# Kernel tuning notes

Measured on AMD Instinct MI355X. Metric: run time of the kernel, lower is better.

Reference implementation:

```python
import jax, jax.numpy as jnp
import numpy as np

VAL_CONF = 0.1
NUM_CLASSES = 80
IMG_SIZE = 608.0


def setup_inputs() -> dict:
    key = jax.random.key(0)
    bs, H, W = 16, 76, 76
    num_mask, attrs = 3, 5 + NUM_CLASSES
    x = jax.random.normal(key, (bs, num_mask * attrs, H, W), dtype=jnp.float32)
    # scaled anchors (anchor_px / img_size) for mask [0,1,2] of YOLOv3 @ 608
    anchors = jnp.array([[10.0, 13.0], [16.0, 30.0], [33.0, 23.0]], dtype=jnp.float32) / IMG_SIZE
    return {"x": x, "anchors": anchors}


def reference(x, anchors):
    # x: [bs, num_mask*(5+nc), H, W]; anchors: [num_mask, 2] (scaled)
    bs, C, H, W = x.shape
    nm = anchors.shape[0]
    attrs = C // nm
    a = x.reshape(bs, nm, attrs, H, W)

    xy = jax.nn.sigmoid(a[:, :, 0:2])          # tx, ty  [bs,nm,2,H,W]
    wh = jnp.exp(a[:, :, 2:4])                 # tw, th
    conf = jax.nn.sigmoid(a[:, :, 4])          # objectness [bs,nm,H,W]
    cls = jax.nn.sigmoid(a[:, :, 5:])          # class probs [bs,nm,nc,H,W]

    gx = jnp.arange(W, dtype=x.dtype)[None, None, None, :]
    gy = jnp.arange(H, dtype=x.dtype)[None, None, :, None]

    cx = (xy[:, :, 0] + gx) / W                # normalized center x
    cy = (xy[:, :, 1] + gy) / H
    bw = wh[:, :, 0] * anchors[None, :, 0, None, None]
    bh = wh[:, :, 1] * anchors[None, :, 1, None, None]

    cls_score = jnp.max(cls, axis=2)           # [bs,nm,H,W]
    cls_idx = jnp.argmax(cls, axis=2).astype(x.dtype)

    # [bs, nm, H, W, 7]: x1,y1,x2,y2,conf,cls_score,cls_idx
    pred = jnp.stack(
        [cx - bw * 0.5, cy - bh * 0.5, cx + bw * 0.5, cy + bh * 0.5,
         conf, cls_score, cls_idx], axis=-1)

    # fixed-shape replacement for the conf>val_conf boolean filter + cat
    valid = conf > VAL_CONF                    # [bs,nm,H,W] bool
    pred = pred * valid[..., None].astype(x.dtype)
    return pred, valid
```

## Files before the change

kernel.cpp:

```cpp
#include <hip/hip_runtime.h>


#define BS    16
#define NM    3
#define NC    80
#define ATTRS (5 + NC)
#define HH    76
#define WW    76
#define HWSZ  (HH * WW)
#define VAL_CONF 0.1f

__device__ __forceinline__ float sigmoidf(float v) {
    return 1.0f / (1.0f + __expf(-v));
}

__global__ __launch_bounds__(256) void yolo_head_kernel(
    const float* __restrict__ x,
    const float* __restrict__ anchors,
    float* __restrict__ out) {

    const int tid = blockIdx.x * blockDim.x + threadIdx.x;

    const int bm = tid / HWSZ;
    const int hw = tid - bm * HWSZ;
    const int m  = bm % NM;

    const float aw = anchors[2 * m + 0];
    const float ah = anchors[2 * m + 1];

    const float* base = x + (size_t)bm * ATTRS * HWSZ + hw;

    const float tx = base[0 * HWSZ];
    const float ty = base[1 * HWSZ];
    const float tw = base[2 * HWSZ];
    const float th = base[3 * HWSZ];
    const float tc = base[4 * HWSZ];

    float mx = base[5 * HWSZ];
    int   mi = 0;
    #pragma unroll
    for (int k = 1; k < NC; ++k) {
        const float c = base[(size_t)(5 + k) * HWSZ];
        if (c > mx) { mx = c; mi = k; }
    }

    const int h = hw / WW;
    const int w = hw - h * WW;

    const float sx = sigmoidf(tx);
    const float sy = sigmoidf(ty);
    const float cx = (sx + (float)w) * (1.0f / (float)WW);
    const float cy = (sy + (float)h) * (1.0f / (float)HH);
    const float bw = __expf(tw) * aw;
    const float bh = __expf(th) * ah;
    const float conf      = sigmoidf(tc);
    const float cls_score = sigmoidf(mx);
    const float cls_idx   = (float)mi;

    const float fm = (conf > VAL_CONF) ? 1.0f : 0.0f;

    float* pred = out + (size_t)tid * 7;
    pred[0] = (cx - bw * 0.5f) * fm;
    pred[1] = (cy - bh * 0.5f) * fm;
    pred[2] = (cx + bw * 0.5f) * fm;
    pred[3] = (cy + bh * 0.5f) * fm;
    pred[4] = conf * fm;
    pred[5] = cls_score * fm;
    pred[6] = cls_idx * fm;

    out[(size_t)BS * NM * HWSZ * 7 + tid] = fm;
}

extern "C" void kernel_launch(void* const* d_in, const int* in_sizes, int n_in,
                              void* d_out, int out_size, void* d_ws, size_t ws_size,
                              hipStream_t stream) {
    const float* x       = (const float*)d_in[0];
    const float* anchors = (const float*)d_in[1];
    float* out           = (float*)d_out;

    const int total = BS * NM * HWSZ;
    const int block = 256;
    const int grid  = total / block;

    yolo_head_kernel<<<grid, block, 0, stream>>>(x, anchors, out);
}
```

Before: 21.95 us.

## Split class argmax across 4-lane groups with float4 loads and shuffle reduce

Each group of four threads now covers four adjacent spatial positions. Each thread loads float4 vectors from a strided subset of the 80 class planes, so it handles 20 classes for all four positions. Partial max/argmax values are then combined with xor shuffles, ties going to the lower index. The aim is fewer, wider load instructions per thread and fewer dependent compares, at the cost of shuffle overhead and extra registers.

```diff
diff --git a/kernel.cpp b/kernel.cpp
--- a/kernel.cpp
+++ b/kernel.cpp
@@ -10,6 +10,8 @@
 #define HWSZ  (HH * WW)
 #define VAL_CONF 0.1f
 
+typedef float f4 __attribute__((ext_vector_type(4)));
+
 __device__ __forceinline__ float sigmoidf(float v) {
     return 1.0f / (1.0f + __expf(-v));
 }
@@ -19,33 +21,56 @@
     const float* __restrict__ anchors,
     float* __restrict__ out) {
 
-    const int tid = blockIdx.x * blockDim.x + threadIdx.x;
+    const int gtid = blockIdx.x * blockDim.x + threadIdx.x;
+    const int t    = gtid & 3;
+    const int e0   = gtid & ~3;
 
-    const int bm = tid / HWSZ;
-    const int hw = tid - bm * HWSZ;
-    const int m  = bm % NM;
+    const int bm  = e0 / HWSZ;
+    const int hw0 = e0 - bm * HWSZ;
+    const int m   = bm % NM;
 
     const float aw = anchors[2 * m + 0];
     const float ah = anchors[2 * m + 1];
 
-    const float* base = x + (size_t)bm * ATTRS * HWSZ + hw;
+    const float* base = x + (size_t)bm * (ATTRS * HWSZ) + hw0;
 
-    const float tx = base[0 * HWSZ];
-    const float ty = base[1 * HWSZ];
-    const float tw = base[2 * HWSZ];
-    const float th = base[3 * HWSZ];
-    const float tc = base[4 * HWSZ];
+    const float tx = base[0 * HWSZ + t];
+    const float ty = base[1 * HWSZ + t];
+    const float tw = base[2 * HWSZ + t];
+    const float th = base[3 * HWSZ + t];
+    const float tc = base[4 * HWSZ + t];
 
-    float mx = base[5 * HWSZ];
-    int   mi = 0;
+    f4  mx = *(const f4*)(base + (size_t)(5 + t) * HWSZ);
+    int mi[4] = {t, t, t, t};
+
     #pragma unroll
-    for (int k = 1; k < NC; ++k) {
-        const float c = base[(size_t)(5 + k) * HWSZ];
-        if (c > mx) { mx = c; mi = k; }
+    for (int i = 1; i < NC / 4; ++i) {
+        const int k = t + 4 * i;
+        const f4 c = *(const f4*)(base + (size_t)(5 + k) * HWSZ);
+        #pragma unroll
+        for (int j = 0; j < 4; ++j) {
+            if (c[j] > mx[j]) { mx[j] = c[j]; mi[j] = k; }
+        }
     }
 
-    const int h = hw / WW;
-    const int w = hw - h * WW;
+    #pragma unroll
+    for (int d = 1; d <= 2; d <<= 1) {
+        #pragma unroll
+        for (int j = 0; j < 4; ++j) {
+            const float omx = __shfl_xor(mx[j], d);
+            const int   omi = __shfl_xor(mi[j], d);
+            if (omx > mx[j] || (omx == mx[j] && omi < mi[j])) {
+                mx[j] = omx; mi[j] = omi;
+            }
+        }
+    }
+
+    const float mxv = (t == 0) ? mx[0] : (t == 1) ? mx[1] : (t == 2) ? mx[2] : mx[3];
+    const int   miv = (t == 0) ? mi[0] : (t == 1) ? mi[1] : (t == 2) ? mi[2] : mi[3];
+
+    const int hw = hw0 + t;
+    const int h  = hw / WW;
+    const int w  = hw - h * WW;
 
     const float sx = sigmoidf(tx);
     const float sy = sigmoidf(ty);
@@ -54,12 +79,12 @@
     const float bw = __expf(tw) * aw;
     const float bh = __expf(th) * ah;
     const float conf      = sigmoidf(tc);
-    const float cls_score = sigmoidf(mx);
-    const float cls_idx   = (float)mi;
+    const float cls_score = sigmoidf(mxv);
+    const float cls_idx   = (float)miv;
 
     const float fm = (conf > VAL_CONF) ? 1.0f : 0.0f;
 
-    float* pred = out + (size_t)tid * 7;
+    float* pred = out + (size_t)gtid * 7;
     pred[0] = (cx - bw * 0.5f) * fm;
     pred[1] = (cy - bh * 0.5f) * fm;
     pred[2] = (cx + bw * 0.5f) * fm;
@@ -68,7 +93,7 @@
     pred[5] = cls_score * fm;
     pred[6] = cls_idx * fm;
 
-    out[(size_t)BS * NM * HWSZ * 7 + tid] = fm;
+    out[(size_t)BS * NM * HWSZ * 7 + gtid] = fm;
 }
 
 extern "C" void kernel_launch(void* const* d_in, const int* in_sizes, int n_in,
```

Result: slower. 22.63 us (+3.1%).
